# Performance work log

Hardware: AMD Instinct MI355X
Metric: run time of the kernel (lower is better)

The kernel has to match this reference:

```python
import jax, jax.numpy as jnp
import numpy as np

INPDIM = 512
RECDIM = 512


def setup_inputs() -> dict:
    key = jax.random.key(0)
    k1, k2, k3, k4 = jax.random.split(key, 4)
    x = jax.random.normal(k1, (64, 1024, INPDIM), dtype=jnp.float32)
    W = jax.random.normal(k2, (INPDIM, RECDIM), dtype=jnp.float32) / np.sqrt(INPDIM)
    # per-unit recurrent weight vector, kept in (-1, 1) for stability
    u = jax.random.uniform(k3, (RECDIM,), dtype=jnp.float32, minval=-1.0, maxval=1.0)
    b = jax.random.normal(k4, (RECDIM,), dtype=jnp.float32) * 0.01
    return {"x": x, "W": W, "u": u, "b": b}


def reference(x, W, u, b):
    # IndRNN: h_t = relu(x_t @ W + u * h_{t-1} + b), h_0 = ones(recdim)
    B, T, _ = x.shape
    # Batch the input projection as one big GEMM (time-independent part).
    xp = jnp.einsum('bti,ir->btr', x, W) + b  # [B, T, R]
    h0 = jnp.ones((B, W.shape[1]), dtype=x.dtype)

    def step(h, xp_t):
        h = jax.nn.relu(xp_t + u * h)
        return h, h

    _, hs = jax.lax.scan(step, h0, jnp.swapaxes(xp, 0, 1))  # hs: [T, B, R]
    return jnp.swapaxes(hs, 0, 1)  # [B, T, R]
```

## Files before the change

kernel.cpp:

```cpp
#include <hip/hip_runtime.h>
#include <hip/hip_fp16.h>
#include <stdint.h>

#define TILE 128
#define BK 32
#define LDST 40

typedef __attribute__((ext_vector_type(8))) short short8;
typedef __attribute__((ext_vector_type(8))) unsigned short ushort8;
typedef __attribute__((ext_vector_type(4))) float f32x4;

static __device__ __forceinline__ unsigned short f2bf(float f) {
    union { float f; uint32_t u; } v; v.f = f;
    uint32_t u = v.u;
    u += 0x7fffu + ((u >> 16) & 1u);
    return (unsigned short)(u >> 16);
}

__global__ __launch_bounds__(256)
void wt_kernel(const float* __restrict__ W, unsigned short* __restrict__ Wt)
{
    __shared__ float s[32][33];
    const int tx = threadIdx.x;
    const int ty = threadIdx.y;
    const int kBase = blockIdx.x * 32;
    const int nBase = blockIdx.y * 32;
    #pragma unroll
    for (int j = 0; j < 4; ++j)
        s[ty + 8 * j][tx] = W[(size_t)(kBase + ty + 8 * j) * 512 + nBase + tx];
    __syncthreads();
    #pragma unroll
    for (int j = 0; j < 4; ++j)
        Wt[(size_t)(nBase + ty + 8 * j) * 512 + kBase + tx] = f2bf(s[tx][ty + 8 * j]);
}

template <bool F16OUT>
__global__ __launch_bounds__(256, 2)
void gemm_bias_kernel(const float* __restrict__ X, const unsigned short* __restrict__ Wt,
                      const float* __restrict__ bias,
                      float* __restrict__ out32, __half* __restrict__ xpT)
{
    __shared__ unsigned short As[TILE * LDST];
    __shared__ unsigned short Bs[TILE * LDST];

    const int tid = threadIdx.x;

    const int lin = blockIdx.x;
    const int xcd = lin & 7;
    const int idx = lin >> 3;
    const int rowBase = (xcd * 64 + (idx >> 2)) * TILE;
    const int colBase = (idx & 3) * TILE;

    const int wave  = tid >> 6;
    const int lane  = tid & 63;
    const int m16   = lane & 15;
    const int quad  = lane >> 4;
    const int waveM = wave & 1;
    const int waveN = wave >> 1;

    f32x4 acc[4][4] = {};

    const int srow = tid >> 2;
    const int sc4  = tid & 3;

    for (int kt = 0; kt < 512; kt += BK) {
        #pragma unroll
        for (int p = 0; p < 2; ++p) {
            int r = p * 64 + srow;
            const float* src = X + (size_t)(rowBase + r) * 512 + kt + sc4 * 8;
            float4 v0 = *(const float4*)(src);
            float4 v1 = *(const float4*)(src + 4);
            ushort8 us;
            us[0] = f2bf(v0.x); us[1] = f2bf(v0.y); us[2] = f2bf(v0.z); us[3] = f2bf(v0.w);
            us[4] = f2bf(v1.x); us[5] = f2bf(v1.y); us[6] = f2bf(v1.z); us[7] = f2bf(v1.w);
            *(ushort8*)(&As[r * LDST + sc4 * 8]) = us;
        }
        #pragma unroll
        for (int p = 0; p < 2; ++p) {
            int n = p * 64 + srow;
            ushort8 v = *(const ushort8*)(Wt + (size_t)(colBase + n) * 512 + kt + sc4 * 8);
            *(ushort8*)(&Bs[n * LDST + sc4 * 8]) = v;
        }
        __syncthreads();

        short8 a_frag[4], b_frag[4];
        #pragma unroll
        for (int mi = 0; mi < 4; ++mi)
            a_frag[mi] = *(const short8*)&As[(waveM * 64 + mi * 16 + m16) * LDST + quad * 8];
        #pragma unroll
        for (int ni = 0; ni < 4; ++ni)
            b_frag[ni] = *(const short8*)&Bs[(waveN * 64 + ni * 16 + m16) * LDST + quad * 8];

        #pragma unroll
        for (int mi = 0; mi < 4; ++mi)
            #pragma unroll
            for (int ni = 0; ni < 4; ++ni) {
                if (F16OUT)
                    acc[mi][ni] = __builtin_amdgcn_mfma_f32_16x16x32_bf16(
                        b_frag[ni], a_frag[mi], acc[mi][ni], 0, 0, 0);
                else
                    acc[mi][ni] = __builtin_amdgcn_mfma_f32_16x16x32_bf16(
                        a_frag[mi], b_frag[ni], acc[mi][ni], 0, 0, 0);
            }
        __syncthreads();
    }

    if (F16OUT) {
        const int bb = rowBase >> 10;
        #pragma unroll
        for (int ni = 0; ni < 4; ++ni) {
            int r0 = colBase + waveN * 64 + ni * 16 + quad * 4;
            float4 b4 = *(const float4*)&bias[r0];
            #pragma unroll
            for (int mi = 0; mi < 4; ++mi) {
                int tt = (rowBase + waveM * 64 + mi * 16 + m16) & 1023;
                #pragma unroll
                for (int r = 0; r < 4; ++r) {
                    float v = acc[mi][ni][r] + ((const float*)&b4)[r];
                    xpT[((size_t)bb * 512 + r0 + r) * 1024 + tt] = __float2half_rn(v);
                }
            }
        }
    } else {
        #pragma unroll
        for (int ni = 0; ni < 4; ++ni) {
            int col = colBase + waveN * 64 + ni * 16 + m16;
            float bv = bias[col];
            #pragma unroll
            for (int mi = 0; mi < 4; ++mi) {
                int row0 = rowBase + waveM * 64 + mi * 16 + quad * 4;
                #pragma unroll
                for (int r = 0; r < 4; ++r) {
                    float v = acc[mi][ni][r] + bv;
                    out32[(size_t)(row0 + r) * 512 + col] = v;
                }
            }
        }
    }
}

#define SUNR 128

__global__ __launch_bounds__(64)
void scan_t_kernel(const __half* __restrict__ xpT, float* __restrict__ out,
                   const float* __restrict__ u)
{
    const int gid = blockIdx.x * 64 + threadIdx.x;
    const int b = gid >> 9;
    const int r = gid & 511;
    const float ur = u[r];
    const unsigned short* p = (const unsigned short*)xpT + ((size_t)b * 512 + r) * 1024;
    float* po = out + (size_t)b * 1024 * 512 + r;

    float h = 1.0f;
    ushort8 cur[SUNR / 8], nxt[SUNR / 8];
    #pragma unroll
    for (int j = 0; j < SUNR / 8; ++j) cur[j] = *(const ushort8*)(p + j * 8);

    for (int t0 = 0; t0 < 1024; t0 += SUNR) {
        const bool more = (t0 + SUNR) < 1024;
        if (more) {
            #pragma unroll
            for (int j = 0; j < SUNR / 8; ++j)
                nxt[j] = *(const ushort8*)(p + t0 + SUNR + j * 8);
        }
        #pragma unroll
        for (int j = 0; j < SUNR / 8; ++j) {
            #pragma unroll
            for (int e = 0; e < 8; ++e) {
                float xv = __half2float(__ushort_as_half(cur[j][e]));
                h = fmaxf(fmaf(ur, h, xv), 0.0f);
                __builtin_nontemporal_store(h, po + (size_t)(t0 + j * 8 + e) * 512);
            }
        }
        #pragma unroll
        for (int j = 0; j < SUNR / 8; ++j) cur[j] = nxt[j];
    }
}

#define UNR 32
__global__ __launch_bounds__(64)
void scan_f32_kernel(float* __restrict__ out, const float* __restrict__ u)
{
    const int gid = blockIdx.x * 64 + threadIdx.x;
    const int b = gid >> 9;
    const int r = gid & 511;
    const float ur = u[r];
    float* p = out + (size_t)b * 1024 * 512 + r;

    float h = 1.0f;
    float cur[UNR], nxt[UNR];
    #pragma unroll
    for (int j = 0; j < UNR; ++j) cur[j] = p[(size_t)j * 512];

    for (int t0 = 0; t0 < 1024; t0 += UNR) {
        const bool more = (t0 + UNR) < 1024;
        const float* pn = p + (size_t)(t0 + UNR) * 512;
        if (more) {
            #pragma unroll
            for (int j = 0; j < UNR; ++j) nxt[j] = pn[(size_t)j * 512];
        }
        #pragma unroll
        for (int j = 0; j < UNR; ++j) {
            h = fmaxf(fmaf(ur, h, cur[j]), 0.0f);
            p[(size_t)(t0 + j) * 512] = h;
        }
        #pragma unroll
        for (int j = 0; j < UNR; ++j) cur[j] = nxt[j];
    }
}

extern "C" void kernel_launch(void* const* d_in, const int* in_sizes, int n_in,
                              void* d_out, int out_size, void* d_ws, size_t ws_size,
                              hipStream_t stream) {
    const float* x = (const float*)d_in[0];
    const float* W = (const float*)d_in[1];
    const float* u = (const float*)d_in[2];
    const float* b = (const float*)d_in[3];
    float* out = (float*)d_out;

    const size_t WT_BYTES = (size_t)512 * 512 * 2;
    const size_t XP_BYTES = (size_t)64 * 1024 * 512 * 2;
    unsigned short* Wt = (unsigned short*)d_ws;
    __half* xp16 = (__half*)((char*)d_ws + WT_BYTES);
    const bool f16path = ws_size >= WT_BYTES + XP_BYTES;

    dim3 tgrid(16, 16), tblk(32, 8);
    wt_kernel<<<tgrid, tblk, 0, stream>>>(W, Wt);

    dim3 grid(2048);
    if (f16path) {
        gemm_bias_kernel<true><<<grid, 256, 0, stream>>>(x, Wt, b, nullptr, xp16);
        scan_t_kernel<<<512, 64, 0, stream>>>(xp16, out, u);
    } else {
        gemm_bias_kernel<false><<<grid, 256, 0, stream>>>(x, Wt, b, out, nullptr);
        scan_f32_kernel<<<512, 64, 0, stream>>>(out, u);
    }
}
```

Measured before the change: 291.5 us.

## Load X tiles directly to LDS as fp32 and tile xpT layout for coalesced scan reads

The GEMM now moves fp32 X straight from global memory into a swizzled shared-memory buffer with global_load_lds. The bf16 conversion happens when the A fragments are read, which removes the register round trip and per-thread conversion on the load path. The fp16 intermediate is written in a blocked layout of 16 timesteps by 64 channels, so each wave in the scan kernel reads contiguous 16-element chunks per lane instead of long strided rows. The trade-off is double the LDS footprint for the A tile and conversion work repeated in every wave that reads each fragment.

```diff
diff --git a/kernel.cpp b/kernel.cpp
--- a/kernel.cpp
+++ b/kernel.cpp
@@ -1,5 +1,6 @@
 #include <hip/hip_runtime.h>
 #include <hip/hip_fp16.h>
+#include <hip/hip_bf16.h>
 #include <stdint.h>
 
 #define TILE 128
@@ -9,6 +10,9 @@
 typedef __attribute__((ext_vector_type(8))) short short8;
 typedef __attribute__((ext_vector_type(8))) unsigned short ushort8;
 typedef __attribute__((ext_vector_type(4))) float f32x4;
+
+typedef const __attribute__((address_space(1))) void* gptr_t;
+typedef __attribute__((address_space(3))) void* lptr_t;
 
 static __device__ __forceinline__ unsigned short f2bf(float f) {
     union { float f; uint32_t u; } v; v.f = f;
@@ -17,6 +21,13 @@
     return (unsigned short)(u >> 16);
 }
 
+static __device__ __forceinline__ unsigned int pk_bf16(float a, float b) {
+    __hip_bfloat162 h = __float22bfloat162_rn(float2{a, b});
+    union { __hip_bfloat162 h; unsigned int u; } c; c.h = h;
+    return c.u;
+}
+
+
 __global__ __launch_bounds__(256)
 void wt_kernel(const float* __restrict__ W, unsigned short* __restrict__ Wt)
 {
@@ -40,7 +51,7 @@
                       const float* __restrict__ bias,
                       float* __restrict__ out32, __half* __restrict__ xpT)
 {
-    __shared__ unsigned short As[TILE * LDST];
+    __shared__ float Asf[TILE * 32];
     __shared__ unsigned short Bs[TILE * LDST];
 
     const int tid = threadIdx.x;
@@ -65,15 +76,14 @@
 
     for (int kt = 0; kt < 512; kt += BK) {
         #pragma unroll
-        for (int p = 0; p < 2; ++p) {
-            int r = p * 64 + srow;
-            const float* src = X + (size_t)(rowBase + r) * 512 + kt + sc4 * 8;
-            float4 v0 = *(const float4*)(src);
-            float4 v1 = *(const float4*)(src + 4);
-            ushort8 us;
-            us[0] = f2bf(v0.x); us[1] = f2bf(v0.y); us[2] = f2bf(v0.z); us[3] = f2bf(v0.w);
-            us[4] = f2bf(v1.x); us[5] = f2bf(v1.y); us[6] = f2bf(v1.z); us[7] = f2bf(v1.w);
-            *(ushort8*)(&As[r * LDST + sc4 * 8]) = us;
+        for (int i = 0; i < 4; ++i) {
+            const int cbase = i * 256 + wave * 64;
+            const int c = cbase + lane;
+            const int m = c >> 3, j = c & 7;
+            const float* src = X + (size_t)(rowBase + m) * 512 + kt + ((j ^ (m & 7)) * 4);
+            __builtin_amdgcn_global_load_lds((gptr_t)src,
+                                             (lptr_t)((char*)Asf + cbase * 16),
+                                             16, 0, 0);
         }
         #pragma unroll
         for (int p = 0; p < 2; ++p) {
@@ -85,8 +95,18 @@
 
         short8 a_frag[4], b_frag[4];
         #pragma unroll
-        for (int mi = 0; mi < 4; ++mi)
-            a_frag[mi] = *(const short8*)&As[(waveM * 64 + mi * 16 + m16) * LDST + quad * 8];
+        for (int mi = 0; mi < 4; ++mi) {
+            int r = waveM * 64 + mi * 16 + m16;
+            const float* rowp = Asf + r * 32;
+            int g0 = (quad * 2)     ^ (r & 7);
+            int g1 = (quad * 2 + 1) ^ (r & 7);
+            float4 fa0 = *(const float4*)(rowp + g0 * 4);
+            float4 fa1 = *(const float4*)(rowp + g1 * 4);
+            union { short8 s8; unsigned int u[4]; } af;
+            af.u[0] = pk_bf16(fa0.x, fa0.y); af.u[1] = pk_bf16(fa0.z, fa0.w);
+            af.u[2] = pk_bf16(fa1.x, fa1.y); af.u[3] = pk_bf16(fa1.z, fa1.w);
+            a_frag[mi] = af.s8;
+        }
         #pragma unroll
         for (int ni = 0; ni < 4; ++ni)
             b_frag[ni] = *(const short8*)&Bs[(waveN * 64 + ni * 16 + m16) * LDST + quad * 8];
@@ -113,11 +133,12 @@
             float4 b4 = *(const float4*)&bias[r0];
             #pragma unroll
             for (int mi = 0; mi < 4; ++mi) {
-                int tt = (rowBase + waveM * 64 + mi * 16 + m16) & 1023;
+                int tc = ((rowBase + waveM * 64 + mi * 16) & 1023) >> 4;
                 #pragma unroll
-                for (int r = 0; r < 4; ++r) {
-                    float v = acc[mi][ni][r] + ((const float*)&b4)[r];
-                    xpT[((size_t)bb * 512 + r0 + r) * 1024 + tt] = __float2half_rn(v);
+                for (int rr = 0; rr < 4; ++rr) {
+                    int r = r0 + rr;
+                    size_t off = ((((size_t)bb * 8 + (r >> 6)) * 64 + tc) * 64 + (r & 63)) * 16 + m16;
+                    xpT[off] = __float2half_rn(acc[mi][ni][rr] + ((const float*)&b4)[rr]);
                 }
             }
         }
@@ -145,27 +166,31 @@
 void scan_t_kernel(const __half* __restrict__ xpT, float* __restrict__ out,
                    const float* __restrict__ u)
 {
-    const int gid = blockIdx.x * 64 + threadIdx.x;
-    const int b = gid >> 9;
-    const int r = gid & 511;
+    const int l  = threadIdx.x;
+    const int b  = blockIdx.x >> 3;
+    const int rg = blockIdx.x & 7;
+    const int r  = rg * 64 + l;
     const float ur = u[r];
-    const unsigned short* p = (const unsigned short*)xpT + ((size_t)b * 512 + r) * 1024;
+    const unsigned short* pt = (const unsigned short*)xpT
+        + ((size_t)(b * 8 + rg) * 64) * 1024 + l * 16;
     float* po = out + (size_t)b * 1024 * 512 + r;
 
     float h = 1.0f;
-    ushort8 cur[SUNR / 8], nxt[SUNR / 8];
-    #pragma unroll
-    for (int j = 0; j < SUNR / 8; ++j) cur[j] = *(const ushort8*)(p + j * 8);
+    ushort8 cur[16], nxt[16];
+    #pragma unroll
+    for (int j = 0; j < 16; ++j)
+        cur[j] = *(const ushort8*)(pt + (j >> 1) * 1024 + (j & 1) * 8);
 
     for (int t0 = 0; t0 < 1024; t0 += SUNR) {
         const bool more = (t0 + SUNR) < 1024;
         if (more) {
-            #pragma unroll
-            for (int j = 0; j < SUNR / 8; ++j)
-                nxt[j] = *(const ushort8*)(p + t0 + SUNR + j * 8);
-        }
-        #pragma unroll
-        for (int j = 0; j < SUNR / 8; ++j) {
+            const unsigned short* pn = pt + (size_t)((t0 + SUNR) >> 4) * 1024;
+            #pragma unroll
+            for (int j = 0; j < 16; ++j)
+                nxt[j] = *(const ushort8*)(pn + (j >> 1) * 1024 + (j & 1) * 8);
+        }
+        #pragma unroll
+        for (int j = 0; j < 16; ++j) {
             #pragma unroll
             for (int e = 0; e < 8; ++e) {
                 float xv = __half2float(__ushort_as_half(cur[j][e]));
@@ -174,7 +199,7 @@
             }
         }
         #pragma unroll
-        for (int j = 0; j < SUNR / 8; ++j) cur[j] = nxt[j];
+        for (int j = 0; j < 16; ++j) cur[j] = nxt[j];
     }
 }
 
```

Measured after the change: 298.7 us. +2.5%, slower.
